# Kernel optimization log

Measured on AMD Instinct MI355X. Metric: run time of the kernel, lower is better.

Reference implementation:

```python
import jax, jax.numpy as jnp
import numpy as np

EPS = 1e-8  # torch F.cosine_similarity default eps


def setup_inputs() -> dict:
    key = jax.random.key(0)
    k1, k2 = jax.random.split(key)
    proto = jax.random.normal(k1, (1, 10, 640, 1, 196), dtype=jnp.float32)
    query = jax.random.normal(k2, (1, 300, 640, 1, 196), dtype=jnp.float32)
    return {"proto": proto, "query": query}


def reference(proto, query):
    # squeeze episode and singleton spatial dims: [way, C, N], [Q, C, N]
    p = proto[0, :, :, 0, :]
    q = query[0, :, :, 0, :]
    # cosine similarity over C between every proto spatial location i and
    # query spatial location j -> sim[q, w, i, j]
    # dots via a single contraction instead of the repeated/broadcast tensors
    dots = jnp.einsum('wci,qcj->qwij', p, q)               # [Q, way, N, N]
    p_norm = jnp.sqrt(jnp.sum(p * p, axis=1))              # [way, N]
    q_norm = jnp.sqrt(jnp.sum(q * q, axis=1))              # [Q, N]
    denom = p_norm[None, :, :, None] * q_norm[:, None, None, :]
    sim = dots / jnp.maximum(denom, EPS)
    return sim
```

## Files before the change

### kernel.cpp

```cpp
#include <hip/hip_runtime.h>
#include <stdint.h>

#define QN    300
#define WN    10
#define CD    640
#define IJ    196
#define MROWS 1960
#define NTOT  58800
#define OUTQ  384160
#define EPSV  1e-8f

#define BM    256
#define BN    256
#define BK    64
#define BUFE  ((BM + BN) * BK)
#define NTK   (CD / BK)

#define MT_TILES 8
#define NT_TILES 230
#define NWG      (MT_TILES * NT_TILES)
#define CPX      (NWG / 8)

typedef __attribute__((ext_vector_type(8))) short bf16x8;
typedef __attribute__((ext_vector_type(4))) float f32x4;

__device__ __forceinline__ unsigned short f2bf(float f) {
    uint32_t u = __float_as_uint(f);
    u += 0x7FFFu + ((u >> 16) & 1u);
    return (unsigned short)(u >> 16);
}

__device__ __forceinline__ void gload16(const void* g, void* l) {
    __builtin_amdgcn_global_load_lds(
        (const __attribute__((address_space(1))) void*)g,
        (__attribute__((address_space(3))) void*)l,
        16, 0, 0);
}

__global__ __launch_bounds__(256)
void prep_all(const float* __restrict__ proto, const float* __restrict__ query,
              uint4* __restrict__ pT, uint4* __restrict__ qT,
              float* __restrict__ pn, float* __restrict__ qn)
{
    __shared__ float T[128][65];
    __shared__ float ssL[64][17];

    const int bi = blockIdx.y;
    const bool isQ = (bi < QN);
    const int b  = isQ ? bi : bi - QN;
    const float* Xb = (isQ ? query : proto) + (size_t)b * (CD * IJ);
    uint4* XT   = isQ ? qT : pT;
    float* nrm  = isQ ? qn : pn;
    const int rowbase = b * IJ;

    const int i0 = blockIdx.x * 64;
    const int t  = threadIdx.x;

    const int cg = t >> 4;
    const int i4 = (t & 15) * 4;
    const int iv = i0 + i4;
    const bool liv = (iv <= IJ - 4);

    const int u   = t & 15;
    const int ilb = (t >> 4) * 4;

    float ss[4] = {0.f, 0.f, 0.f, 0.f};

    for (int cc = 0; cc < CD / 128; ++cc) {
        #pragma unroll
        for (int pass = 0; pass < 8; ++pass) {
            int cl = pass * 16 + cg;
            int c  = cc * 128 + cl;
            float4 v = make_float4(0.f, 0.f, 0.f, 0.f);
            if (liv) v = *(const float4*)&Xb[(size_t)c * IJ + iv];
            T[cl][i4 + 0] = v.x; T[cl][i4 + 1] = v.y;
            T[cl][i4 + 2] = v.z; T[cl][i4 + 3] = v.w;
        }
        __syncthreads();
        #pragma unroll
        for (int j = 0; j < 4; ++j) {
            int il = ilb + j;
            float v[8];
            #pragma unroll
            for (int r = 0; r < 8; ++r) { v[r] = T[u * 8 + r][il]; ss[j] += v[r] * v[r]; }
            int ig = i0 + il;
            if (ig < IJ) {
                union { unsigned short s[8]; uint4 q; } pk;
                #pragma unroll
                for (int r = 0; r < 8; ++r) pk.s[r] = f2bf(v[r]);
                int rowg = rowbase + ig;
                int us = (u & 8) | ((u & 7) ^ (rowg & 7));
                XT[(size_t)rowg * (CD / 8) + cc * 16 + us] = pk.q;
            }
        }
        __syncthreads();
    }

    #pragma unroll
    for (int j = 0; j < 4; ++j) ssL[ilb + j][u] = ss[j];
    __syncthreads();
    if (t < 64) {
        int ig = i0 + t;
        if (ig < IJ) {
            float s = 0.f;
            #pragma unroll
            for (int k = 0; k < 16; ++k) s += ssL[t][k];
            nrm[rowbase + ig] = sqrtf(s);
        }
    }
}

__global__ __launch_bounds__(512, 2)
void gemm_kernel(const uint4* __restrict__ AT, const uint4* __restrict__ BT,
                 const float* __restrict__ pn, const float* __restrict__ qn,
                 float* __restrict__ out)
{
    __shared__ unsigned short lds[2 * BUFE];

    const int bid = blockIdx.x;
    const int swz = (bid & 7) * CPX + (bid >> 3);
    const int mt  = swz & (MT_TILES - 1);
    const int nt  = swz >> 3;
    const int m0  = mt * BM;
    const int n0  = nt * BN;

    const int t  = threadIdx.x;
    const int w  = t >> 6, l = t & 63;
    const int fr = l & 15, fq = l >> 4;
    const int wm0 = (w >> 2) * 128;
    const int wn0 = (w & 3) * 64;

    const int lr = l >> 3, lu = l & 7;
    int ra00 = m0 +   0 + w * 8 + lr; if (ra00 > MROWS - 1) ra00 = MROWS - 1;
    int ra01 = m0 +  64 + w * 8 + lr; if (ra01 > MROWS - 1) ra01 = MROWS - 1;
    int ra10 = m0 + 128 + w * 8 + lr; if (ra10 > MROWS - 1) ra10 = MROWS - 1;
    int ra11 = m0 + 192 + w * 8 + lr; if (ra11 > MROWS - 1) ra11 = MROWS - 1;
    int rb00 = n0 +   0 + w * 8 + lr; if (rb00 > NTOT - 1) rb00 = NTOT - 1;
    int rb01 = n0 +  64 + w * 8 + lr; if (rb01 > NTOT - 1) rb01 = NTOT - 1;
    int rb10 = n0 + 128 + w * 8 + lr; if (rb10 > NTOT - 1) rb10 = NTOT - 1;
    int rb11 = n0 + 192 + w * 8 + lr; if (rb11 > NTOT - 1) rb11 = NTOT - 1;
    const uint4* ga00 = AT + (size_t)ra00 * 80 + lu;
    const uint4* ga01 = AT + (size_t)ra01 * 80 + lu;
    const uint4* ga10 = AT + (size_t)ra10 * 80 + lu;
    const uint4* ga11 = AT + (size_t)ra11 * 80 + lu;
    const uint4* gb00 = BT + (size_t)rb00 * 80 + lu;
    const uint4* gb01 = BT + (size_t)rb01 * 80 + lu;
    const uint4* gb10 = BT + (size_t)rb10 * 80 + lu;
    const uint4* gb11 = BT + (size_t)rb11 * 80 + lu;
    const int la00 = (  0 + w * 8) * 64;
    const int la01 = ( 64 + w * 8) * 64;
    const int la10 = (128 + w * 8) * 64;
    const int la11 = (192 + w * 8) * 64;
    const int lb00 = BM * 64 + (  0 + w * 8) * 64;
    const int lb01 = BM * 64 + ( 64 + w * 8) * 64;
    const int lb10 = BM * 64 + (128 + w * 8) * 64;
    const int lb11 = BM * 64 + (192 + w * 8) * 64;

    const int fqS0 = fq << 3;
    const int fqS1 = (fq + 4) << 3;
    int baA[8], kyA[8], baB[4], kyB[4];
    #pragma unroll
    for (int i = 0; i < 8; ++i) {
        int rowa = wm0 + i * 16 + fr;
        baA[i] = rowa * 64;  kyA[i] = (rowa & 7) << 3;
    }
    #pragma unroll
    for (int i = 0; i < 4; ++i) {
        int rowb = wn0 + i * 16 + fr;
        baB[i] = BM * 64 + rowb * 64;  kyB[i] = (rowb & 7) << 3;
    }

    f32x4 acc[8][4];
    #pragma unroll
    for (int a = 0; a < 8; ++a)
        #pragma unroll
        for (int bb = 0; bb < 4; ++bb)
            acc[a][bb] = (f32x4){0.f, 0.f, 0.f, 0.f};

#define ST2(PA, PB, LA, LB)                                               \
    gload16(PA, (char*)&lds[(LA)]); PA += 8;                              \
    gload16(PB, (char*)&lds[(LB)]); PB += 8;

#define RD_A(OC, G)                                                       \
    _Pragma("unroll")                                                     \
    for (int mm = 0; mm < 4; ++mm) {                                      \
        af[mm]   = *(const bf16x8*)&lds[(OC) + baA[(G)+mm]                \
                                        + (fqS0 ^ kyA[(G)+mm])];          \
        af[4+mm] = *(const bf16x8*)&lds[(OC) + baA[(G)+mm]                \
                                        + (fqS1 ^ kyA[(G)+mm])];          \
    }
#define RD_B(BV, OC, G)                                                   \
    _Pragma("unroll")                                                     \
    for (int nn = 0; nn < 2; ++nn) {                                      \
        BV[nn]   = *(const bf16x8*)&lds[(OC) + baB[(G)+nn]                \
                                        + (fqS0 ^ kyB[(G)+nn])];          \
        BV[2+nn] = *(const bf16x8*)&lds[(OC) + baB[(G)+nn]                \
                                        + (fqS1 ^ kyB[(G)+nn])];          \
    }
#define MF(MB, NB, BV)                                                    \
    _Pragma("unroll")                                                     \
    for (int ks = 0; ks < 2; ++ks)                                        \
        _Pragma("unroll")                                                 \
        for (int mm = 0; mm < 4; ++mm)                                    \
            _Pragma("unroll")                                             \
            for (int nn = 0; nn < 2; ++nn)                                \
                acc[(MB)+mm][(NB)+nn] =                                   \
                    __builtin_amdgcn_mfma_f32_16x16x32_bf16(              \
                        BV[ks*2+nn], af[ks*4+mm],                         \
                        acc[(MB)+mm][(NB)+nn], 0, 0, 0);

#define BAR    __builtin_amdgcn_s_barrier()
#define LGKM0  do { asm volatile("s_waitcnt lgkmcnt(0)" ::: "memory");    \
                    __builtin_amdgcn_sched_barrier(0); } while (0)
#define VMC(N) asm volatile("s_waitcnt vmcnt(" #N ")" ::: "memory")
#define PRIO1  __builtin_amdgcn_s_setprio(1)
#define PRIO0  __builtin_amdgcn_s_setprio(0)

    ST2(ga00, ga01, la00, la01);
    ST2(gb00, gb01, lb00, lb01);
    ST2(ga10, ga11, la10, la11);
    ST2(gb10, gb11, lb10, lb11);
    ST2(ga00, ga01, BUFE + la00, BUFE + la01);
    VMC(2); BAR;

    for (int i5 = 0; i5 < NTK / 2; ++i5) {
        bf16x8 af[8], b0[4], b1[4];
        RD_A(0, 0); RD_B(b0, 0, 0);
        ST2(gb00, gb01, BUFE + lb00, BUFE + lb01);
        BAR; LGKM0;
        PRIO1; MF(0, 0, b0); PRIO0;
        RD_B(b1, 0, 2);
        ST2(ga10, ga11, BUFE + la10, BUFE + la11);
        BAR; LGKM0;
        PRIO1; MF(0, 2, b1); PRIO0;
        RD_A(0, 4);
        ST2(gb10, gb11, BUFE + lb10, BUFE + lb11);
        BAR; LGKM0;
        PRIO1; MF(4, 2, b1); PRIO0;
        ST2(ga00, ga01, la00, la01);
        PRIO1; MF(4, 0, b0); PRIO0;
        VMC(2); BAR;
        RD_A(BUFE, 0); RD_B(b0, BUFE, 0);
        ST2(gb00, gb01, lb00, lb01);
        BAR; LGKM0;
        PRIO1; MF(0, 0, b0); PRIO0;
        RD_B(b1, BUFE, 2);
        ST2(ga10, ga11, la10, la11);
        BAR; LGKM0;
        PRIO1; MF(0, 2, b1); PRIO0;
        RD_A(BUFE, 4);
        ST2(gb10, gb11, lb10, lb11);
        BAR; LGKM0;
        PRIO1; MF(4, 2, b1); PRIO0;
        ST2(ga00, ga01, BUFE + la00, BUFE + la01);
        PRIO1; MF(4, 0, b0); PRIO0;
        VMC(2); BAR;
    }

    VMC(0);

#undef ST2
#undef RD_A
#undef RD_B
#undef MF
#undef BAR
#undef LGKM0
#undef VMC
#undef PRIO1
#undef PRIO0

    float4 rqv4[4];
    int    nok[4];
    size_t ob[4];
    #pragma unroll
    for (int tn = 0; tn < 4; ++tn) {
        int n = n0 + wn0 + tn * 16 + fq * 4;
        nok[tn] = (n < NTOT);
        int nc = nok[tn] ? n : NTOT - 4;
        int q  = nc / IJ;
        int j  = nc - q * IJ;
        rqv4[tn] = *(const float4*)&qn[nc];
        ob[tn] = (size_t)q * OUTQ + j;
    }
    #pragma unroll
    for (int tm = 0; tm < 8; ++tm) {
        int m = m0 + wm0 + tm * 16 + fr;
        if (m < MROWS) {
            float rp = pn[m];
            #pragma unroll
            for (int tn = 0; tn < 4; ++tn) {
                if (nok[tn]) {
                    f32x4 a = acc[tm][tn];
                    float4 o;
                    o.x = a[0] * __builtin_amdgcn_rcpf(fmaxf(rp * rqv4[tn].x, EPSV));
                    o.y = a[1] * __builtin_amdgcn_rcpf(fmaxf(rp * rqv4[tn].y, EPSV));
                    o.z = a[2] * __builtin_amdgcn_rcpf(fmaxf(rp * rqv4[tn].z, EPSV));
                    o.w = a[3] * __builtin_amdgcn_rcpf(fmaxf(rp * rqv4[tn].w, EPSV));
                    *(float4*)&out[ob[tn] + (size_t)m * IJ] = o;
                }
            }
        }
    }
}

#define BMF 128
#define BNF 224
#define LPAD 40
__global__ __launch_bounds__(512, 4)
void sim_fallback(const float* __restrict__ proto,
                  const float* __restrict__ query,
                  float* __restrict__ out)
{
    __shared__ unsigned short As[BMF][LPAD];
    __shared__ unsigned short Bs[BNF][LPAD];
    __shared__ float redA[4][BMF];
    __shared__ float redB[2][BNF];
    __shared__ float rpS[BMF];
    __shared__ float rqS[BNF];

    const int tid = threadIdx.x;
    const int m0  = blockIdx.x * BMF;
    const int q   = blockIdx.y;

    const int mA  = tid & (BMF - 1);
    const int krA = tid >> 7;
    const int wiA = m0 + mA;
    const bool va = (wiA < MROWS);
    const int wA  = va ? (wiA / IJ) : 0;
    const int iA  = va ? (wiA - wA * IJ) : 0;
    const float* pA = proto + wA * (CD * IJ) + iA;

    const bool tb  = (tid < 448);
    const int jB   = tb ? (tid % BNF) : 0;
    const int krB  = tb ? (tid / BNF) : 0;
    const bool vb  = tb && (jB < IJ);
    const float* qB = query + q * (CD * IJ) + jB;

    float ssA = 0.f, ssB = 0.f;

    const int wv   = tid >> 6;
    const int lane = tid & 63;
    const int wm0  = (wv >> 1) * 32;
    const int wn0  = (wv & 1) * 112;
    const int fr   = lane & 15;
    const int fq   = lane >> 4;

    f32x4 acc[2][7];
    #pragma unroll
    for (int a = 0; a < 2; a++)
        #pragma unroll
        for (int b = 0; b < 7; b++)
            acc[a][b] = (f32x4){0.f, 0.f, 0.f, 0.f};

    for (int it = 0; it < CD / 32; ++it) {
        const int c0 = it * 32;
        {
            float v[8];
            #pragma unroll
            for (int e = 0; e < 8; e++) {
                int c = c0 + krA * 8 + e;
                v[e] = va ? pA[c * IJ] : 0.f;
            }
            #pragma unroll
            for (int e = 0; e < 8; e++) ssA += v[e] * v[e];
            union { unsigned short s[8]; uint4 u; } pk;
            #pragma unroll
            for (int e = 0; e < 8; e++) pk.s[e] = f2bf(v[e]);
            *(uint4*)&As[mA][krA * 8] = pk.u;
        }
        if (tb) {
            #pragma unroll
            for (int h = 0; h < 2; ++h) {
                float v[8];
                #pragma unroll
                for (int e = 0; e < 8; e++) {
                    int c = c0 + krB * 16 + h * 8 + e;
                    v[e] = vb ? qB[c * IJ] : 0.f;
                }
                #pragma unroll
                for (int e = 0; e < 8; e++) ssB += v[e] * v[e];
                union { unsigned short s[8]; uint4 u; } pk;
                #pragma unroll
                for (int e = 0; e < 8; e++) pk.s[e] = f2bf(v[e]);
                *(uint4*)&Bs[jB][krB * 16 + h * 8] = pk.u;
            }
        }
        __syncthreads();
        bf16x8 af[2], bfv[7];
        #pragma unroll
        for (int tm = 0; tm < 2; tm++)
            af[tm] = *(const bf16x8*)&As[wm0 + tm * 16 + fr][fq * 8];
        #pragma unroll
        for (int tn = 0; tn < 7; tn++)
            bfv[tn] = *(const bf16x8*)&Bs[wn0 + tn * 16 + fr][fq * 8];
        #pragma unroll
        for (int tm = 0; tm < 2; tm++)
            #pragma unroll
            for (int tn = 0; tn < 7; tn++)
                acc[tm][tn] = __builtin_amdgcn_mfma_f32_16x16x32_bf16(
                    af[tm], bfv[tn], acc[tm][tn], 0, 0, 0);
        __syncthreads();
    }

    redA[krA][mA] = ssA;
    if (tb) redB[krB][jB] = ssB;
    __syncthreads();
    if (tid < BMF) {
        rpS[tid] = sqrtf(redA[0][tid] + redA[1][tid] + redA[2][tid] + redA[3][tid]);
    } else if (tid >= 256 && tid < 256 + BNF) {
        int j = tid - 256;
        rqS[j] = sqrtf(redB[0][j] + redB[1][j]);
    }
    __syncthreads();

    #pragma unroll
    for (int tm = 0; tm < 2; tm++) {
        #pragma unroll
        for (int tn = 0; tn < 7; tn++) {
            #pragma unroll
            for (int r = 0; r < 4; r++) {
                int rl = wm0 + tm * 16 + fq * 4 + r;
                int cl = wn0 + tn * 16 + fr;
                int wi = m0 + rl;
                if (wi < MROWS && cl < IJ) {
                    float denom = fmaxf(rpS[rl] * rqS[cl], 1e-8f);
                    out[(size_t)(q * MROWS + wi) * IJ + cl] = acc[tm][tn][r] / denom;
                }
            }
        }
    }
}

extern "C" void kernel_launch(void* const* d_in, const int* in_sizes, int n_in,
                              void* d_out, int out_size, void* d_ws, size_t ws_size,
                              hipStream_t stream) {
    const float* proto = (const float*)d_in[0];
    const float* query = (const float*)d_in[1];
    float* out = (float*)d_out;

    const size_t off_pT = 0;
    const size_t off_qT = 2508800;
    const size_t off_pn = 77772800;
    const size_t off_qn = 77780736;
    const size_t need   = 78015936;

    if (ws_size < need) {
        dim3 grid((MROWS + BMF - 1) / BMF, QN);
        sim_fallback<<<grid, 512, 0, stream>>>(proto, query, out);
        return;
    }

    char* ws = (char*)d_ws;
    uint4* pT = (uint4*)(ws + off_pT);
    uint4* qT = (uint4*)(ws + off_qT);
    float* pn = (float*)(ws + off_pn);
    float* qn = (float*)(ws + off_qn);

    prep_all<<<dim3(4, QN + WN), 256, 0, stream>>>(proto, query, pT, qT, pn, qn);

    gemm_kernel<<<dim3(NWG), 512, 0, stream>>>(pT, qT, pn, qn, out);
}
```

Before: 353.2 us.

## Load A fragments directly from global into registers, stage only B via 4-deep LDS ring

The GEMM main loop is restructured. A-operand fragments (prototype rows, a small matrix reused by all tiles) are now read straight from global memory into registers and double-buffered there. Only the B tile is staged through LDS, using a 4-slot ring with BK reduced to 32. The pre-transpose swizzle is changed to match the new 4-chunk-per-row layout. This cuts LDS footprint and LDS read traffic and simplifies barriers, but it relies on A fragments hitting cache, and each A load now comes from global memory with higher latency, gated by vmcnt counts.

Result: slower. 447.1 us (+26.6%).

```diff
diff --git a/kernel.cpp b/kernel.cpp
--- a/kernel.cpp
+++ b/kernel.cpp
@@ -12,9 +12,9 @@
 
 #define BM    256
 #define BN    256
-#define BK    64
-#define BUFE  ((BM + BN) * BK)
+#define BK    32
 #define NTK   (CD / BK)
+#define BUFB  8192
 
 #define MT_TILES 8
 #define NT_TILES 230
@@ -89,7 +89,7 @@
                 #pragma unroll
                 for (int r = 0; r < 8; ++r) pk.s[r] = f2bf(v[r]);
                 int rowg = rowbase + ig;
-                int us = (u & 8) | ((u & 7) ^ (rowg & 7));
+                int us = (u & 12) | ((u & 3) ^ ((rowg >> 1) & 3));
                 XT[(size_t)rowg * (CD / 8) + cc * 16 + us] = pk.q;
             }
         }
@@ -115,7 +115,7 @@
                  const float* __restrict__ pn, const float* __restrict__ qn,
                  float* __restrict__ out)
 {
-    __shared__ unsigned short lds[2 * BUFE];
+    __shared__ unsigned short lds[4 * BUFB];
 
     const int bid = blockIdx.x;
     const int swz = (bid & 7) * CPX + (bid >> 3);
@@ -130,44 +130,27 @@
     const int wm0 = (w >> 2) * 128;
     const int wn0 = (w & 3) * 64;
 
-    const int lr = l >> 3, lu = l & 7;
-    int ra00 = m0 +   0 + w * 8 + lr; if (ra00 > MROWS - 1) ra00 = MROWS - 1;
-    int ra01 = m0 +  64 + w * 8 + lr; if (ra01 > MROWS - 1) ra01 = MROWS - 1;
-    int ra10 = m0 + 128 + w * 8 + lr; if (ra10 > MROWS - 1) ra10 = MROWS - 1;
-    int ra11 = m0 + 192 + w * 8 + lr; if (ra11 > MROWS - 1) ra11 = MROWS - 1;
-    int rb00 = n0 +   0 + w * 8 + lr; if (rb00 > NTOT - 1) rb00 = NTOT - 1;
-    int rb01 = n0 +  64 + w * 8 + lr; if (rb01 > NTOT - 1) rb01 = NTOT - 1;
-    int rb10 = n0 + 128 + w * 8 + lr; if (rb10 > NTOT - 1) rb10 = NTOT - 1;
-    int rb11 = n0 + 192 + w * 8 + lr; if (rb11 > NTOT - 1) rb11 = NTOT - 1;
-    const uint4* ga00 = AT + (size_t)ra00 * 80 + lu;
-    const uint4* ga01 = AT + (size_t)ra01 * 80 + lu;
-    const uint4* ga10 = AT + (size_t)ra10 * 80 + lu;
-    const uint4* ga11 = AT + (size_t)ra11 * 80 + lu;
-    const uint4* gb00 = BT + (size_t)rb00 * 80 + lu;
-    const uint4* gb01 = BT + (size_t)rb01 * 80 + lu;
-    const uint4* gb10 = BT + (size_t)rb10 * 80 + lu;
-    const uint4* gb11 = BT + (size_t)rb11 * 80 + lu;
-    const int la00 = (  0 + w * 8) * 64;
-    const int la01 = ( 64 + w * 8) * 64;
-    const int la10 = (128 + w * 8) * 64;
-    const int la11 = (192 + w * 8) * 64;
-    const int lb00 = BM * 64 + (  0 + w * 8) * 64;
-    const int lb01 = BM * 64 + ( 64 + w * 8) * 64;
-    const int lb10 = BM * 64 + (128 + w * 8) * 64;
-    const int lb11 = BM * 64 + (192 + w * 8) * 64;
-
-    const int fqS0 = fq << 3;
-    const int fqS1 = (fq + 4) << 3;
-    int baA[8], kyA[8], baB[4], kyB[4];
+    const int srow = w * 16 + (l >> 2);
+    const int su   = l & 3;
+    int rb0 = n0 +       srow; if (rb0 > NTOT - 1) rb0 = NTOT - 1;
+    int rb1 = n0 + 128 + srow; if (rb1 > NTOT - 1) rb1 = NTOT - 1;
+    const uint4* gb0 = BT + (size_t)rb0 * 80 + su;
+    const uint4* gb1 = BT + (size_t)rb1 * 80 + su;
+    const int lb0 = w * 512;
+    const int lb1 = 4096 + w * 512;
+
+    const uint4* pa[8];
     #pragma unroll
     for (int i = 0; i < 8; ++i) {
-        int rowa = wm0 + i * 16 + fr;
-        baA[i] = rowa * 64;  kyA[i] = (rowa & 7) << 3;
-    }
+        int row = m0 + wm0 + i * 16 + fr; if (row > MROWS - 1) row = MROWS - 1;
+        pa[i] = AT + (size_t)row * 80 + (fq ^ ((row >> 1) & 3));
+    }
+
+    int foB[4];
     #pragma unroll
     for (int i = 0; i < 4; ++i) {
-        int rowb = wn0 + i * 16 + fr;
-        baB[i] = BM * 64 + rowb * 64;  kyB[i] = (rowb & 7) << 3;
+        int row = wn0 + i * 16 + fr;
+        foB[i] = row * 32 + ((fq ^ ((row >> 1) & 3)) << 3);
     }
 
     f32x4 acc[8][4];
@@ -177,94 +160,55 @@
         for (int bb = 0; bb < 4; ++bb)
             acc[a][bb] = (f32x4){0.f, 0.f, 0.f, 0.f};
 
-#define ST2(PA, PB, LA, LB)                                               \
-    gload16(PA, (char*)&lds[(LA)]); PA += 8;                              \
-    gload16(PB, (char*)&lds[(LB)]); PB += 8;
-
-#define RD_A(OC, G)                                                       \
+#define STB(BUF)                                                          \
+    gload16(gb0, (char*)&lds[(BUF) * BUFB + lb0]); gb0 += 4;              \
+    gload16(gb1, (char*)&lds[(BUF) * BUFB + lb1]); gb1 += 4;
+
+#define LDA(AF)                                                           \
     _Pragma("unroll")                                                     \
-    for (int mm = 0; mm < 4; ++mm) {                                      \
-        af[mm]   = *(const bf16x8*)&lds[(OC) + baA[(G)+mm]                \
-                                        + (fqS0 ^ kyA[(G)+mm])];          \
-        af[4+mm] = *(const bf16x8*)&lds[(OC) + baA[(G)+mm]                \
-                                        + (fqS1 ^ kyA[(G)+mm])];          \
-    }
-#define RD_B(BV, OC, G)                                                   \
-    _Pragma("unroll")                                                     \
-    for (int nn = 0; nn < 2; ++nn) {                                      \
-        BV[nn]   = *(const bf16x8*)&lds[(OC) + baB[(G)+nn]                \
-                                        + (fqS0 ^ kyB[(G)+nn])];          \
-        BV[2+nn] = *(const bf16x8*)&lds[(OC) + baB[(G)+nn]                \
-                                        + (fqS1 ^ kyB[(G)+nn])];          \
-    }
-#define MF(MB, NB, BV)                                                    \
-    _Pragma("unroll")                                                     \
-    for (int ks = 0; ks < 2; ++ks)                                        \
-        _Pragma("unroll")                                                 \
-        for (int mm = 0; mm < 4; ++mm)                                    \
-            _Pragma("unroll")                                             \
-            for (int nn = 0; nn < 2; ++nn)                                \
-                acc[(MB)+mm][(NB)+nn] =                                   \
-                    __builtin_amdgcn_mfma_f32_16x16x32_bf16(              \
-                        BV[ks*2+nn], af[ks*4+mm],                         \
-                        acc[(MB)+mm][(NB)+nn], 0, 0, 0);
+    for (int i = 0; i < 8; ++i) { AF[i] = *(const bf16x8*)pa[i]; pa[i] += 4; }
 
 #define BAR    __builtin_amdgcn_s_barrier()
-#define LGKM0  do { asm volatile("s_waitcnt lgkmcnt(0)" ::: "memory");    \
-                    __builtin_amdgcn_sched_barrier(0); } while (0)
+#define SBAR0  __builtin_amdgcn_sched_barrier(0)
 #define VMC(N) asm volatile("s_waitcnt vmcnt(" #N ")" ::: "memory")
 #define PRIO1  __builtin_amdgcn_s_setprio(1)
 #define PRIO0  __builtin_amdgcn_s_setprio(0)
 
-    ST2(ga00, ga01, la00, la01);
-    ST2(gb00, gb01, lb00, lb01);
-    ST2(ga10, ga11, la10, la11);
-    ST2(gb10, gb11, lb10, lb11);
-    ST2(ga00, ga01, BUFE + la00, BUFE + la01);
-    VMC(2); BAR;
-
-    for (int i5 = 0; i5 < NTK / 2; ++i5) {
-        bf16x8 af[8], b0[4], b1[4];
-        RD_A(0, 0); RD_B(b0, 0, 0);
-        ST2(gb00, gb01, BUFE + lb00, BUFE + lb01);
-        BAR; LGKM0;
-        PRIO1; MF(0, 0, b0); PRIO0;
-        RD_B(b1, 0, 2);
-        ST2(ga10, ga11, BUFE + la10, BUFE + la11);
-        BAR; LGKM0;
-        PRIO1; MF(0, 2, b1); PRIO0;
-        RD_A(0, 4);
-        ST2(gb10, gb11, BUFE + lb10, BUFE + lb11);
-        BAR; LGKM0;
-        PRIO1; MF(4, 2, b1); PRIO0;
-        ST2(ga00, ga01, la00, la01);
-        PRIO1; MF(4, 0, b0); PRIO0;
-        VMC(2); BAR;
-        RD_A(BUFE, 0); RD_B(b0, BUFE, 0);
-        ST2(gb00, gb01, lb00, lb01);
-        BAR; LGKM0;
-        PRIO1; MF(0, 0, b0); PRIO0;
-        RD_B(b1, BUFE, 2);
-        ST2(ga10, ga11, la10, la11);
-        BAR; LGKM0;
-        PRIO1; MF(0, 2, b1); PRIO0;
-        RD_A(BUFE, 4);
-        ST2(gb10, gb11, lb10, lb11);
-        BAR; LGKM0;
-        PRIO1; MF(4, 2, b1); PRIO0;
-        ST2(ga00, ga01, BUFE + la00, BUFE + la01);
-        PRIO1; MF(4, 0, b0); PRIO0;
-        VMC(2); BAR;
+#define PH(BUF, AFC, AFN)                                                 \
+  { STB((BUF + 2) & 3); LDA(AFN);                                         \
+    VMC(10); BAR; SBAR0;                                                  \
+    bf16x8 bf[4];                                                         \
+    _Pragma("unroll")                                                     \
+    for (int nf = 0; nf < 4; ++nf)                                        \
+        bf[nf] = *(const bf16x8*)&lds[(BUF) * BUFB + foB[nf]];            \
+    PRIO1;                                                                \
+    _Pragma("unroll")                                                     \
+    for (int mm = 0; mm < 8; ++mm)                                        \
+        _Pragma("unroll")                                                 \
+        for (int nn = 0; nn < 4; ++nn)                                    \
+            acc[mm][nn] = __builtin_amdgcn_mfma_f32_16x16x32_bf16(        \
+                bf[nn], AFC[mm], acc[mm][nn], 0, 0, 0);                   \
+    PRIO0; }
+
+    bf16x8 afA[8], afB[8];
+
+    STB(0); STB(1); LDA(afA);
+    VMC(8); BAR;
+
+    for (int it = 0; it < 5; ++it) {
+        PH(0, afA, afB)
+        PH(1, afB, afA)
+        PH(2, afA, afB)
+        PH(3, afB, afA)
     }
 
     VMC(0);
 
-#undef ST2
-#undef RD_A
-#undef RD_B
-#undef MF
+#undef PH
+#undef STB
+#undef LDA
 #undef BAR
-#undef LGKM0
+#undef SBAR0
 #undef VMC
 #undef PRIO1
 #undef PRIO0
```

## Make GEMM kernel persistent and prefetch next tile during last K iteration

Applied to the files above, without the earlier changes.

The GEMM launch becomes persistent: 256 workgroups each loop over 7 or 8 output tiles instead of one workgroup per tile. The global-to-LDS loads for the next tile's first K-slab are issued in the final K iteration of the current tile, so the next tile's loads can overlap the current tile's epilogue. This removes per-workgroup launch and pipeline-fill costs and hides prologue latency. The fixed grid of 256 assumes one workgroup per CU, and the 7/8 tile split can leave some CUs idle at the end.

Result: slower. 479.9 us (+35.9%).

```diff
diff --git a/kernel.cpp b/kernel.cpp
--- a/kernel.cpp
+++ b/kernel.cpp
@@ -20,6 +20,7 @@
 #define NT_TILES 230
 #define NWG      (MT_TILES * NT_TILES)
 #define CPX      (NWG / 8)
+#define PBLK     256
 
 typedef __attribute__((ext_vector_type(8))) short bf16x8;
 typedef __attribute__((ext_vector_type(4))) float f32x4;
@@ -117,36 +118,16 @@
 {
     __shared__ unsigned short lds[2 * BUFE];
 
-    const int bid = blockIdx.x;
-    const int swz = (bid & 7) * CPX + (bid >> 3);
-    const int mt  = swz & (MT_TILES - 1);
-    const int nt  = swz >> 3;
-    const int m0  = mt * BM;
-    const int n0  = nt * BN;
+    const int b   = blockIdx.x;
+    const int cnt = (b < NWG - 7 * PBLK) ? 8 : 7;
 
     const int t  = threadIdx.x;
     const int w  = t >> 6, l = t & 63;
     const int fr = l & 15, fq = l >> 4;
     const int wm0 = (w >> 2) * 128;
     const int wn0 = (w & 3) * 64;
-
     const int lr = l >> 3, lu = l & 7;
-    int ra00 = m0 +   0 + w * 8 + lr; if (ra00 > MROWS - 1) ra00 = MROWS - 1;
-    int ra01 = m0 +  64 + w * 8 + lr; if (ra01 > MROWS - 1) ra01 = MROWS - 1;
-    int ra10 = m0 + 128 + w * 8 + lr; if (ra10 > MROWS - 1) ra10 = MROWS - 1;
-    int ra11 = m0 + 192 + w * 8 + lr; if (ra11 > MROWS - 1) ra11 = MROWS - 1;
-    int rb00 = n0 +   0 + w * 8 + lr; if (rb00 > NTOT - 1) rb00 = NTOT - 1;
-    int rb01 = n0 +  64 + w * 8 + lr; if (rb01 > NTOT - 1) rb01 = NTOT - 1;
-    int rb10 = n0 + 128 + w * 8 + lr; if (rb10 > NTOT - 1) rb10 = NTOT - 1;
-    int rb11 = n0 + 192 + w * 8 + lr; if (rb11 > NTOT - 1) rb11 = NTOT - 1;
-    const uint4* ga00 = AT + (size_t)ra00 * 80 + lu;
-    const uint4* ga01 = AT + (size_t)ra01 * 80 + lu;
-    const uint4* ga10 = AT + (size_t)ra10 * 80 + lu;
-    const uint4* ga11 = AT + (size_t)ra11 * 80 + lu;
-    const uint4* gb00 = BT + (size_t)rb00 * 80 + lu;
-    const uint4* gb01 = BT + (size_t)rb01 * 80 + lu;
-    const uint4* gb10 = BT + (size_t)rb10 * 80 + lu;
-    const uint4* gb11 = BT + (size_t)rb11 * 80 + lu;
+
     const int la00 = (  0 + w * 8) * 64;
     const int la01 = ( 64 + w * 8) * 64;
     const int la10 = (128 + w * 8) * 64;
@@ -170,12 +151,25 @@
         baB[i] = BM * 64 + rowb * 64;  kyB[i] = (rowb & 7) << 3;
     }
 
+#define SETPA(P, RB) { int r_ = (RB) + w * 8 + lr;                        \
+    if (r_ > MROWS - 1) r_ = MROWS - 1;                                   \
+    P = AT + (size_t)r_ * 80 + lu; }
+#define SETPB(P, RB) { int r_ = (RB) + w * 8 + lr;                        \
+    if (r_ > NTOT - 1) r_ = NTOT - 1;                                     \
+    P = BT + (size_t)r_ * 80 + lu; }
+
+    int v   = b;
+    int szv = (v & 7) * CPX + (v >> 3);
+    int m0  = (szv & (MT_TILES - 1)) * BM;
+    int n0  = (szv >> 3) * BN;
+
+    const uint4 *ga00, *ga01, *ga10, *ga11, *gb00, *gb01, *gb10, *gb11;
+    SETPA(ga00, m0 +   0); SETPA(ga01, m0 +  64);
+    SETPA(ga10, m0 + 128); SETPA(ga11, m0 + 192);
+    SETPB(gb00, n0 +   0); SETPB(gb01, n0 +  64);
+    SETPB(gb10, n0 + 128); SETPB(gb11, n0 + 192);
+
     f32x4 acc[8][4];
-    #pragma unroll
-    for (int a = 0; a < 8; ++a)
-        #pragma unroll
-        for (int bb = 0; bb < 4; ++bb)
-            acc[a][bb] = (f32x4){0.f, 0.f, 0.f, 0.f};
 
 #define ST2(PA, PB, LA, LB)                                               \
     gload16(PA, (char*)&lds[(LA)]); PA += 8;                              \
@@ -216,6 +210,57 @@
 #define PRIO1  __builtin_amdgcn_s_setprio(1)
 #define PRIO0  __builtin_amdgcn_s_setprio(0)
 
+#define ITER(R4, R5, R6, R7)                                              \
+  { bf16x8 af[8], b0[4], b1[4];                                           \
+                                                                  \
+    RD_A(0, 0); RD_B(b0, 0, 0);                                           \
+    ST2(gb00, gb01, BUFE + lb00, BUFE + lb01);                            \
+    BAR; LGKM0;                                                           \
+    PRIO1; MF(0, 0, b0); PRIO0;                                           \
+                                                                  \
+    RD_B(b1, 0, 2);                                                       \
+    ST2(ga10, ga11, BUFE + la10, BUFE + la11);                            \
+    BAR; LGKM0;                                                           \
+    PRIO1; MF(0, 2, b1); PRIO0;                                           \
+                                                                  \
+    RD_A(0, 4);                                                           \
+    ST2(gb10, gb11, BUFE + lb10, BUFE + lb11);                            \
+    BAR; LGKM0;                                                           \
+    PRIO1; MF(4, 2, b1); PRIO0;                                           \
+                                                           \
+    R4;                                                                   \
+    ST2(ga00, ga01, la00, la01);                                          \
+    PRIO1; MF(4, 0, b0); PRIO0;                                           \
+    VMC(2); BAR;                                                          \
+                                                                  \
+    RD_A(BUFE, 0); RD_B(b0, BUFE, 0);                                     \
+    R5;                                                                   \
+    ST2(gb00, gb01, lb00, lb01);                                          \
+    BAR; LGKM0;                                                           \
+    PRIO1; MF(0, 0, b0); PRIO0;                                           \
+                                                                  \
+    RD_B(b1, BUFE, 2);                                                    \
+    R6;                                                                   \
+    ST2(ga10, ga11, la10, la11);                                          \
+    BAR; LGKM0;                                                           \
+    PRIO1; MF(0, 2, b1); PRIO0;                                           \
+                                                                  \
+    RD_A(BUFE, 4);                                                        \
+    R7;                                                                   \
+    ST2(gb10, gb11, lb10, lb11);                                          \
+    BAR; LGKM0;                                                           \
+    PRIO1; MF(4, 2, b1); PRIO0;                                           \
+                                                           \
+    ST2(ga00, ga01, BUFE + la00, BUFE + la01);                            \
+    PRIO1; MF(4, 0, b0); PRIO0;                                           \
+    VMC(2); BAR; }
+
+#define NOP_    do {} while (0)
+#define RST_A0  do { SETPA(ga00, m0n +   0); SETPA(ga01, m0n +  64); } while (0)
+#define RST_B0  do { SETPB(gb00, n0n +   0); SETPB(gb01, n0n +  64); } while (0)
+#define RST_A1  do { SETPA(ga10, m0n + 128); SETPA(ga11, m0n + 192); } while (0)
+#define RST_B1  do { SETPB(gb10, n0n + 128); SETPB(gb11, n0n + 192); } while (0)
+
     ST2(ga00, ga01, la00, la01);
     ST2(gb00, gb01, lb00, lb01);
     ST2(ga10, ga11, la10, la11);
@@ -223,42 +268,69 @@
     ST2(ga00, ga01, BUFE + la00, BUFE + la01);
     VMC(2); BAR;
 
-    for (int i5 = 0; i5 < NTK / 2; ++i5) {
-        bf16x8 af[8], b0[4], b1[4];
-        RD_A(0, 0); RD_B(b0, 0, 0);
-        ST2(gb00, gb01, BUFE + lb00, BUFE + lb01);
-        BAR; LGKM0;
-        PRIO1; MF(0, 0, b0); PRIO0;
-        RD_B(b1, 0, 2);
-        ST2(ga10, ga11, BUFE + la10, BUFE + la11);
-        BAR; LGKM0;
-        PRIO1; MF(0, 2, b1); PRIO0;
-        RD_A(0, 4);
-        ST2(gb10, gb11, BUFE + lb10, BUFE + lb11);
-        BAR; LGKM0;
-        PRIO1; MF(4, 2, b1); PRIO0;
-        ST2(ga00, ga01, la00, la01);
-        PRIO1; MF(4, 0, b0); PRIO0;
-        VMC(2); BAR;
-        RD_A(BUFE, 0); RD_B(b0, BUFE, 0);
-        ST2(gb00, gb01, lb00, lb01);
-        BAR; LGKM0;
-        PRIO1; MF(0, 0, b0); PRIO0;
-        RD_B(b1, BUFE, 2);
-        ST2(ga10, ga11, la10, la11);
-        BAR; LGKM0;
-        PRIO1; MF(0, 2, b1); PRIO0;
-        RD_A(BUFE, 4);
-        ST2(gb10, gb11, lb10, lb11);
-        BAR; LGKM0;
-        PRIO1; MF(4, 2, b1); PRIO0;
-        ST2(ga00, ga01, BUFE + la00, BUFE + la01);
-        PRIO1; MF(4, 0, b0); PRIO0;
-        VMC(2); BAR;
+    for (int k = 0; k < cnt; ++k) {
+        #pragma unroll
+        for (int a = 0; a < 8; ++a)
+            #pragma unroll
+            for (int bb = 0; bb < 4; ++bb)
+                acc[a][bb] = (f32x4){0.f, 0.f, 0.f, 0.f};
+
+        for (int i5 = 0; i5 < 4; ++i5) {
+            ITER(NOP_, NOP_, NOP_, NOP_)
+        }
+
+        int vn  = (k + 1 < cnt) ? v + PBLK : v;
+        int szn = (vn & 7) * CPX + (vn >> 3);
+        int m0n = (szn & (MT_TILES - 1)) * BM;
+        int n0n = (szn >> 3) * BN;
+        ITER(RST_A0, RST_B0, RST_A1, RST_B1)
+
+        {
+            float4 rqv4[4];
+            int    nok[4];
+            size_t ob[4];
+            #pragma unroll
+            for (int tn = 0; tn < 4; ++tn) {
+                int n = n0 + wn0 + tn * 16 + fq * 4;
+                nok[tn] = (n < NTOT);
+                int nc = nok[tn] ? n : NTOT - 4;
+                int q  = nc / IJ;
+                int j  = nc - q * IJ;
+                rqv4[tn] = *(const float4*)&qn[nc];
+                ob[tn] = (size_t)q * OUTQ + j;
+            }
+            #pragma unroll
+            for (int tm = 0; tm < 8; ++tm) {
+                int m = m0 + wm0 + tm * 16 + fr;
+                if (m < MROWS) {
+                    float rp = pn[m];
+                    #pragma unroll
+                    for (int tn = 0; tn < 4; ++tn) {
+                        if (nok[tn]) {
+                            f32x4 a = acc[tm][tn];
+                            float4 o;
+                            o.x = a[0] * __builtin_amdgcn_rcpf(fmaxf(rp * rqv4[tn].x, EPSV));
+                            o.y = a[1] * __builtin_amdgcn_rcpf(fmaxf(rp * rqv4[tn].y, EPSV));
+                            o.z = a[2] * __builtin_amdgcn_rcpf(fmaxf(rp * rqv4[tn].z, EPSV));
+                            o.w = a[3] * __builtin_amdgcn_rcpf(fmaxf(rp * rqv4[tn].w, EPSV));
+                            *(float4*)&out[ob[tn] + (size_t)m * IJ] = o;
+                        }
+                    }
+                }
+            }
+        }
+
+        v = vn; m0 = m0n; n0 = n0n;
     }
 
     VMC(0);
 
+#undef ITER
+#undef NOP_
+#undef RST_A0
+#undef RST_B0
+#undef RST_A1
+#undef RST_B1
 #undef ST2
 #undef RD_A
 #undef RD_B
@@ -268,39 +340,8 @@
 #undef VMC
 #undef PRIO1
 #undef PRIO0
-
-    float4 rqv4[4];
-    int    nok[4];
-    size_t ob[4];
-    #pragma unroll
-    for (int tn = 0; tn < 4; ++tn) {
-        int n = n0 + wn0 + tn * 16 + fq * 4;
-        nok[tn] = (n < NTOT);
-        int nc = nok[tn] ? n : NTOT - 4;
-        int q  = nc / IJ;
-        int j  = nc - q * IJ;
-        rqv4[tn] = *(const float4*)&qn[nc];
-        ob[tn] = (size_t)q * OUTQ + j;
-    }
-    #pragma unroll
-    for (int tm = 0; tm < 8; ++tm) {
-        int m = m0 + wm0 + tm * 16 + fr;
-        if (m < MROWS) {
-            float rp = pn[m];
-            #pragma unroll
-            for (int tn = 0; tn < 4; ++tn) {
-                if (nok[tn]) {
-                    f32x4 a = acc[tm][tn];
-                    float4 o;
-                    o.x = a[0] * __builtin_amdgcn_rcpf(fmaxf(rp * rqv4[tn].x, EPSV));
-                    o.y = a[1] * __builtin_amdgcn_rcpf(fmaxf(rp * rqv4[tn].y, EPSV));
-                    o.z = a[2] * __builtin_amdgcn_rcpf(fmaxf(rp * rqv4[tn].z, EPSV));
-                    o.w = a[3] * __builtin_amdgcn_rcpf(fmaxf(rp * rqv4[tn].w, EPSV));
-                    *(float4*)&out[ob[tn] + (size_t)m * IJ] = o;
-                }
-            }
-        }
-    }
+#undef SETPA
+#undef SETPB
 }
 
 #define BMF 128
@@ -458,5 +499,5 @@
 
     prep_all<<<dim3(4, QN + WN), 256, 0, stream>>>(proto, query, pT, qT, pn, qn);
 
-    gemm_kernel<<<dim3(NWG), 512, 0, stream>>>(pT, qT, pn, qn, out);
+    gemm_kernel<<<dim3(PBLK), 512, 0, stream>>>(pT, qT, pn, qn, out);
 }
```
